# Optimization experiments

Hardware: AMD Instinct MI355X
Metric: run time of the kernel (lower is better)

Reference implementation:

```python
import jax, jax.numpy as jnp
import numpy as np

DIM = 512
NUM_HEADS = 8
HEAD_DIM = DIM // NUM_HEADS
SCALE = HEAD_DIM ** -0.5


def setup_inputs() -> dict:
    key = jax.random.key(0)
    k_x, k_qkv, k_proj, k_pb = jax.random.split(key, 4)
    x = jax.random.normal(k_x, (2, 4096, DIM), dtype=jnp.float32)
    # nn.Linear weights: stored as [out, in]; qkv_bias=False so no qkv bias.
    w_qkv = jax.random.normal(k_qkv, (3 * DIM, DIM), dtype=jnp.float32) * (DIM ** -0.5)
    w_proj = jax.random.normal(k_proj, (DIM, DIM), dtype=jnp.float32) * (DIM ** -0.5)
    b_proj = jax.random.normal(k_pb, (DIM,), dtype=jnp.float32) * 0.01
    return {"x": x, "w_qkv": w_qkv, "w_proj": w_proj, "b_proj": b_proj}


def reference(x, w_qkv, w_proj, b_proj):
    B, N, D = x.shape
    H, Hd = NUM_HEADS, HEAD_DIM
    # qkv: [B, N, 3D] -> [3, B, H, N, Hd]
    qkv = (x @ w_qkv.T).reshape(B, N, 3, H, Hd).transpose(2, 0, 3, 1, 4)
    q, k, v = qkv[0], qkv[1], qkv[2]
    # Naive full attention matrix in fp32 (matches original non-fused path).
    attn = jnp.einsum('bhqd,bhkd->bhqk', q, k) * SCALE
    attn = jax.nn.softmax(attn, axis=-1)
    out = jnp.einsum('bhqk,bhkd->bhqd', attn, v)
    out = out.transpose(0, 2, 1, 3).reshape(B, N, D)
    return out @ w_proj.T + b_proj
```

## Files before the change

### kernel.cpp

```cpp
#include <hip/hip_runtime.h>
#include <stdint.h>

#define SEQ   4096
#define DIMM  512
#define HDIM  64
#define NH    8
#define ROWS  8192
#define QKVN  1536

typedef __attribute__((ext_vector_type(8))) __bf16 bf16x8;
typedef __attribute__((ext_vector_type(4))) float  f32x4;
typedef __attribute__((ext_vector_type(2))) uint32_t u32x2;

__device__ __forceinline__ uint32_t cvtpk(float lo, float hi) {
  uint32_t w;
  asm("v_cvt_pk_bf16_f32 %0, %1, %2" : "=v"(w) : "v"(lo), "v"(hi));
  return w;
}

__device__ __forceinline__ f32x4 mfma16(bf16x8 a, bf16x8 b, f32x4 c) {
  return __builtin_amdgcn_mfma_f32_16x16x32_bf16(a, b, c, 0, 0, 0);
}

#if __has_builtin(__builtin_amdgcn_exp2f)
#define EXP2F(x) __builtin_amdgcn_exp2f(x)
#else
#define EXP2F(x) exp2f(x)
#endif

__device__ __forceinline__ void gld16(const void* g, void* l) {
  __builtin_amdgcn_global_load_lds(
      (const __attribute__((address_space(1))) uint32_t*)g,
      (__attribute__((address_space(3))) uint32_t*)l, 16, 0, 0);
}

#define X4  (ROWS * DIMM / 4)
#define Q4  (QKVN * DIMM / 4)
#define P4  (DIMM * DIMM / 4)

__global__ __launch_bounds__(256) void cvt_kernel(
    const float* __restrict__ x, const float* __restrict__ wq,
    const float* __restrict__ wp, uint16_t* __restrict__ xb,
    uint16_t* __restrict__ wqb, uint16_t* __restrict__ wpb) {
  int idx = blockIdx.x * 256 + threadIdx.x;
  const float* src; uint16_t* dst; int i4;
  if (idx < X4)            { src = x;  dst = xb;  i4 = idx; }
  else if (idx < X4 + Q4)  { src = wq; dst = wqb; i4 = idx - X4; }
  else                     { src = wp; dst = wpb; i4 = idx - X4 - Q4; }
  float4 v = ((const float4*)src)[i4];
  uint2 o;
  o.x = cvtpk(v.x, v.y);
  o.y = cvtpk(v.z, v.w);
  ((uint2*)dst)[i4] = o;
}

__device__ __forceinline__ void gemm_core(
    const uint16_t* __restrict__ A, const uint16_t* __restrict__ B,
    uint16_t* As, uint16_t* Bs, f32x4 acc[4][4]) {
  const int tid = threadIdx.x;
  const int lane = tid & 63, wave = tid >> 6;
  const int quad = lane >> 4, l16 = lane & 15;
  const int wr = (wave & 1) * 64, wc = (wave >> 1) * 64;
  const int bm = blockIdx.x, bn = blockIdx.y;
  const int sw = (l16 >> 1) & 3;

  for (int kt = 0; kt < DIMM / 32; ++kt) {
#pragma unroll
    for (int it = 0; it < 2; ++it) {
      int L = it * 256 + tid;
      int r = L >> 2, c = L & 3;
      int gc = c ^ ((r >> 1) & 3);
      int ldsoff = (it * 256 + (tid & ~63)) * 16;
      gld16((const char*)A + ((size_t)(bm * 128 + r) * DIMM + kt * 32) * 2 + gc * 16,
            (char*)As + ldsoff);
      gld16((const char*)B + ((size_t)(bn * 128 + r) * DIMM + kt * 32) * 2 + gc * 16,
            (char*)Bs + ldsoff);
    }
    __syncthreads();
    bf16x8 af[4], bfr[4];
#pragma unroll
    for (int i = 0; i < 4; ++i)
      af[i] = *(const bf16x8*)(As + (wr + i * 16 + l16) * 32 + ((quad ^ sw) * 8));
#pragma unroll
    for (int j = 0; j < 4; ++j)
      bfr[j] = *(const bf16x8*)(Bs + (wc + j * 16 + l16) * 32 + ((quad ^ sw) * 8));
#pragma unroll
    for (int i = 0; i < 4; ++i)
#pragma unroll
      for (int j = 0; j < 4; ++j)
        acc[i][j] = mfma16(af[i], bfr[j], acc[i][j]);
    __syncthreads();
  }
}

__global__ __launch_bounds__(256, 2) void qkv_gemm(
    const uint16_t* __restrict__ xb, const uint16_t* __restrict__ wqb,
    uint16_t* __restrict__ qd, uint16_t* __restrict__ kd,
    uint16_t* __restrict__ vt) {
  __shared__ __align__(16) uint16_t As[128 * 32];
  __shared__ __align__(16) uint16_t Bs[128 * 32];
  f32x4 acc[4][4];
#pragma unroll
  for (int i = 0; i < 4; ++i)
#pragma unroll
    for (int j = 0; j < 4; ++j) acc[i][j] = f32x4{0.f, 0.f, 0.f, 0.f};

  gemm_core(xb, wqb, As, Bs, acc);

  const int lane = threadIdx.x & 63, wave = threadIdx.x >> 6;
  const int quad = lane >> 4, l16 = lane & 15;
  const int wr = (wave & 1) * 64, wc = (wave >> 1) * 64;
  const float qscale = 0.125f * 1.44269504f;
#pragma unroll
  for (int i = 0; i < 4; ++i) {
    int m0 = blockIdx.x * 128 + wr + i * 16 + quad * 4;
    int b = m0 >> 12, n0 = m0 & 4095;
#pragma unroll
    for (int j = 0; j < 4; ++j) {
      int jc = blockIdx.y * 128 + wc + j * 16 + l16;
      int region = jc >> 9;
      int h = (jc >> 6) & 7, hd = jc & 63;
      int bh = (b << 3) | h;
      if (region == 0) {
        uint32_t w01 = cvtpk(acc[i][j][0] * qscale, acc[i][j][1] * qscale);
        uint32_t w23 = cvtpk(acc[i][j][2] * qscale, acc[i][j][3] * qscale);
        size_t rb = ((size_t)bh * SEQ + n0) * HDIM + hd;
        qd[rb]            = (uint16_t)w01;
        qd[rb + HDIM]     = (uint16_t)(w01 >> 16);
        qd[rb + 2 * HDIM] = (uint16_t)w23;
        qd[rb + 3 * HDIM] = (uint16_t)(w23 >> 16);
      } else if (region == 1) {
        uint32_t w01 = cvtpk(acc[i][j][0], acc[i][j][1]);
        uint32_t w23 = cvtpk(acc[i][j][2], acc[i][j][3]);
        size_t rb = ((size_t)bh * SEQ + n0) * HDIM + hd;
        kd[rb]            = (uint16_t)w01;
        kd[rb + HDIM]     = (uint16_t)(w01 >> 16);
        kd[rb + 2 * HDIM] = (uint16_t)w23;
        kd[rb + 3 * HDIM] = (uint16_t)(w23 >> 16);
      } else {
        uint2 pk;
        pk.x = cvtpk(acc[i][j][0], acc[i][j][1]);
        pk.y = cvtpk(acc[i][j][2], acc[i][j][3]);
        *(uint2*)(vt + ((size_t)bh * HDIM + hd) * SEQ + n0) = pk;
      }
    }
  }
}

__global__ __launch_bounds__(512, 4) void attn_kernel(
    const uint16_t* __restrict__ qd, const uint16_t* __restrict__ kd,
    const uint16_t* __restrict__ vt, uint16_t* __restrict__ ao) {
  __shared__ __align__(16) uint16_t Ks[128 * 64];
  __shared__ __align__(16) uint16_t Vs[64 * 128];
  __shared__ __align__(16) uint16_t Ps[8][32 * 64];

  const int tid = threadIdx.x, lane = tid & 63, wave = tid >> 6;
  const int quad = lane >> 4, l16 = lane & 15;
  const int pair = wave >> 1, khalf = wave & 1;
  const int wid = blockIdx.x;
  const int xcd = wid & 7, slot = wid >> 3;
  const int bh = xcd + 8 * (slot & 1);
  const int qt = slot >> 1;
  const size_t base_qk = (size_t)bh * SEQ * HDIM;
  const size_t base_v  = (size_t)bh * HDIM * SEQ;
  const int sw7 = l16 & 7;
  char* Pw = (char*)Ps + wave * 4096;

  bf16x8 qf[2][2];
#pragma unroll
  for (int it2 = 0; it2 < 2; ++it2)
#pragma unroll
    for (int kh = 0; kh < 2; ++kh)
      qf[it2][kh] = *(const bf16x8*)(qd + base_qk +
          (size_t)(qt * 128 + pair * 32 + it2 * 16 + l16) * HDIM + kh * 32 + quad * 8);

  f32x4 O[2][4];
  float lsum[2] = {0.f, 0.f};
#pragma unroll
  for (int a = 0; a < 2; ++a)
#pragma unroll
    for (int d = 0; d < 4; ++d) O[a][d] = f32x4{0.f, 0.f, 0.f, 0.f};

  for (int kt = 0; kt < SEQ / 128; ++kt) {
#pragma unroll
    for (int it = 0; it < 2; ++it) {
      int L = it * 512 + tid;
      int ldsoff = (it * 512 + (tid & ~63)) * 16;
      int rk = L >> 3, ck = L & 7;
      int gck = ck ^ (rk & 7);
      gld16((const char*)kd + (base_qk + (size_t)(kt * 128 + rk) * HDIM) * 2 + gck * 16,
            (char*)Ks + ldsoff);
      int rv = L >> 4, cv = L & 15;
      int gcv = cv ^ (rv & 15);
      gld16((const char*)vt + (base_v + (size_t)rv * SEQ + (size_t)kt * 128) * 2 + gcv * 16,
            (char*)Vs + ldsoff);
    }
    __syncthreads();

    bf16x8 kf[4][2];
#pragma unroll
    for (int jh = 0; jh < 4; ++jh) {
      int jf = khalf * 4 + jh;
      const uint16_t* krow = Ks + (jf * 16 + l16) * 64;
      kf[jh][0] = *(const bf16x8*)(krow + ((quad ^ sw7) * 8));
      kf[jh][1] = *(const bf16x8*)(krow + (((4 + quad) ^ sw7) * 8));
    }
    f32x4 P[4][2];
    __builtin_amdgcn_s_setprio(1);
#pragma unroll
    for (int jh = 0; jh < 4; ++jh)
#pragma unroll
      for (int it2 = 0; it2 < 2; ++it2) {
        f32x4 s = f32x4{0.f, 0.f, 0.f, 0.f};
        s = mfma16(kf[jh][0], qf[it2][0], s);
        s = mfma16(kf[jh][1], qf[it2][1], s);
        P[jh][it2] = s;
      }
    __builtin_amdgcn_s_setprio(0);

#pragma unroll
    for (int jh = 0; jh < 4; ++jh)
#pragma unroll
      for (int it2 = 0; it2 < 2; ++it2) {
        float p0 = EXP2F(P[jh][it2][0]);
        float p1 = EXP2F(P[jh][it2][1]);
        float p2 = EXP2F(P[jh][it2][2]);
        float p3 = EXP2F(P[jh][it2][3]);
        lsum[it2] += (p0 + p1) + (p2 + p3);
        u32x2 pk;
        pk.x = cvtpk(p0, p1);
        pk.y = cvtpk(p2, p3);
        int c16 = (jh * 2 + (quad >> 1)) ^ sw7;
        *(u32x2*)(Pw + (it2 * 16 + l16) * 128 + c16 * 16 + (quad & 1) * 8) = pk;
      }

#pragma unroll
    for (int kp = 0; kp < 2; ++kp) {
      bf16x8 pb[2];
#pragma unroll
      for (int it2 = 0; it2 < 2; ++it2)
        pb[it2] = *(const bf16x8*)(Pw + (it2 * 16 + l16) * 128 +
                                   (((kp * 4 + quad) ^ sw7) * 16));
      bf16x8 va[4];
#pragma unroll
      for (int dl = 0; dl < 4; ++dl)
        va[dl] = *(const bf16x8*)((const char*)Vs + (dl * 16 + l16) * 256 +
                                  (((khalf * 8 + kp * 4 + quad) ^ l16) & 15) * 16);
      __builtin_amdgcn_s_setprio(1);
#pragma unroll
      for (int it2 = 0; it2 < 2; ++it2)
#pragma unroll
        for (int dl = 0; dl < 4; ++dl)
          O[it2][dl] = mfma16(va[dl], pb[it2], O[it2][dl]);
      __builtin_amdgcn_s_setprio(0);
    }
    __syncthreads();
  }

  if (!(wave & 1)) {
    f32x4* ob = (f32x4*)((char*)Ps + wave * 4096);
#pragma unroll
    for (int it2 = 0; it2 < 2; ++it2)
#pragma unroll
      for (int dl = 0; dl < 4; ++dl)
        ob[(it2 * 4 + dl) * 64 + lane] = O[it2][dl];
    float2* lb = (float2*)((char*)Ks + pair * 512);
    lb[lane] = make_float2(lsum[0], lsum[1]);
  }
  __syncthreads();
  if (wave & 1) {
    const f32x4* ob = (const f32x4*)((char*)Ps + (wave - 1) * 4096);
    float2 lp = ((const float2*)((char*)Ks + pair * 512))[lane];
    lsum[0] += lp.x; lsum[1] += lp.y;
#pragma unroll
    for (int it2 = 0; it2 < 2; ++it2)
#pragma unroll
      for (int dl = 0; dl < 4; ++dl)
        O[it2][dl] += ob[(it2 * 4 + dl) * 64 + lane];

    const int b = bh >> 3, h = bh & 7;
#pragma unroll
    for (int it2 = 0; it2 < 2; ++it2) {
      float l = lsum[it2];
      l += __shfl_xor(l, 16);
      l += __shfl_xor(l, 32);
      float inv = 1.0f / l;
      int q = qt * 128 + pair * 32 + it2 * 16 + l16;
      size_t rowbase = ((size_t)(b * SEQ + q)) * DIMM + h * HDIM;
#pragma unroll
      for (int dl = 0; dl < 4; ++dl) {
        uint2 pk;
        pk.x = cvtpk(O[it2][dl][0] * inv, O[it2][dl][1] * inv);
        pk.y = cvtpk(O[it2][dl][2] * inv, O[it2][dl][3] * inv);
        *(uint2*)(ao + rowbase + dl * 16 + quad * 4) = pk;
      }
    }
  }
}

__global__ __launch_bounds__(256, 2) void proj_gemm(
    const uint16_t* __restrict__ ao, const uint16_t* __restrict__ wpb,
    const float* __restrict__ bprj, float* __restrict__ out) {
  __shared__ __align__(16) uint16_t As[128 * 32];
  __shared__ __align__(16) uint16_t Bs[128 * 32];
  f32x4 acc[4][4];
#pragma unroll
  for (int i = 0; i < 4; ++i)
#pragma unroll
    for (int j = 0; j < 4; ++j) acc[i][j] = f32x4{0.f, 0.f, 0.f, 0.f};

  gemm_core(ao, wpb, As, Bs, acc);

  const int lane = threadIdx.x & 63, wave = threadIdx.x >> 6;
  const int quad = lane >> 4, l16 = lane & 15;
  const int wr = (wave & 1) * 64, wc = (wave >> 1) * 64;
#pragma unroll
  for (int i = 0; i < 4; ++i) {
    int m0 = blockIdx.x * 128 + wr + i * 16 + quad * 4;
#pragma unroll
    for (int j = 0; j < 4; ++j) {
      int jc = blockIdx.y * 128 + wc + j * 16 + l16;
      float bias = bprj[jc];
#pragma unroll
      for (int r = 0; r < 4; ++r)
        out[(size_t)(m0 + r) * DIMM + jc] = acc[i][j][r] + bias;
    }
  }
}

extern "C" void kernel_launch(void* const* d_in, const int* in_sizes, int n_in,
                              void* d_out, int out_size, void* d_ws, size_t ws_size,
                              hipStream_t stream) {
  const float* x     = (const float*)d_in[0];
  const float* wqkv  = (const float*)d_in[1];
  const float* wproj = (const float*)d_in[2];
  const float* bproj = (const float*)d_in[3];

  char* ws = (char*)d_ws;
  uint16_t* xb  = (uint16_t*)(ws + 0);
  uint16_t* wqb = (uint16_t*)(ws + 8388608);
  uint16_t* wpb = (uint16_t*)(ws + 9961472);
  uint16_t* qd  = (uint16_t*)(ws + 10485760);
  uint16_t* kd  = (uint16_t*)(ws + 18874368);
  uint16_t* vt  = (uint16_t*)(ws + 27262976);
  uint16_t* ao  = (uint16_t*)(ws + 35651584);

  cvt_kernel<<<(X4 + Q4 + P4) / 256, 256, 0, stream>>>(x, wqkv, wproj, xb, wqb, wpb);
  qkv_gemm<<<dim3(64, 12), 256, 0, stream>>>(xb, wqb, qd, kd, vt);
  attn_kernel<<<512, 512, 0, stream>>>(qd, kd, vt, ao);
  proj_gemm<<<dim3(64, 4), 256, 0, stream>>>(ao, wpb, bproj, (float*)d_out);
}
```

Before: 183.2 us.

## Double-buffer LDS tiles and keep P in registers via 16x16x16 MFMA

Both GEMMs and the attention kernel now double-buffer their LDS tiles. The next tile's global-to-LDS load is issued right after the barrier, so it overlaps compute on the current tile, and one barrier per iteration is dropped. In attention, the softmax probabilities are packed straight into registers and consumed by a 16x16x16 bf16 MFMA, removing the P round-trip through LDS; the freed Ps space goes toward the extra K/V buffers. The GEMMs also raise the launch-bounds occupancy hint to 4 blocks and add setprio around the MFMA block. The trade-offs are more LDS per block and more, smaller MFMA instructions on the PV step.

```diff
diff --git a/kernel.cpp b/kernel.cpp
--- a/kernel.cpp
+++ b/kernel.cpp
@@ -9,7 +9,9 @@
 #define QKVN  1536
 
 typedef __attribute__((ext_vector_type(8))) __bf16 bf16x8;
+typedef __attribute__((ext_vector_type(4))) __bf16 bf16x4;
 typedef __attribute__((ext_vector_type(4))) float  f32x4;
+typedef __attribute__((ext_vector_type(4))) short  s16x4;
 typedef __attribute__((ext_vector_type(2))) uint32_t u32x2;
 
 __device__ __forceinline__ uint32_t cvtpk(float lo, float hi) {
@@ -20,6 +22,20 @@
 
 __device__ __forceinline__ f32x4 mfma16(bf16x8 a, bf16x8 b, f32x4 c) {
   return __builtin_amdgcn_mfma_f32_16x16x32_bf16(a, b, c, 0, 0, 0);
+}
+
+__device__ __forceinline__ f32x4 pv_mfma(s16x4 a, s16x4 b, f32x4 c) {
+#if __has_builtin(__builtin_amdgcn_mfma_f32_16x16x16bf16_1k)
+  return __builtin_amdgcn_mfma_f32_16x16x16bf16_1k(a, b, c, 0, 0, 0);
+#elif __has_builtin(__builtin_amdgcn_mfma_f32_16x16x16_bf16)
+  return __builtin_amdgcn_mfma_f32_16x16x16_bf16(
+      __builtin_bit_cast(bf16x4, a), __builtin_bit_cast(bf16x4, b), c, 0, 0, 0);
+#else
+  f32x4 d = c;
+  asm volatile("v_mfma_f32_16x16x16_bf16 %0, %1, %2, %3"
+               : "=v"(d) : "v"(a), "v"(b), "0"(d));
+  return d;
+#endif
 }
 
 #if __has_builtin(__builtin_amdgcn_exp2f)
@@ -56,7 +72,7 @@
 
 __device__ __forceinline__ void gemm_core(
     const uint16_t* __restrict__ A, const uint16_t* __restrict__ B,
-    uint16_t* As, uint16_t* Bs, f32x4 acc[4][4]) {
+    uint16_t (*As)[128 * 32], uint16_t (*Bs)[128 * 32], f32x4 acc[4][4]) {
   const int tid = threadIdx.x;
   const int lane = tid & 63, wave = tid >> 6;
   const int quad = lane >> 4, l16 = lane & 15;
@@ -64,7 +80,7 @@
   const int bm = blockIdx.x, bn = blockIdx.y;
   const int sw = (l16 >> 1) & 3;
 
-  for (int kt = 0; kt < DIMM / 32; ++kt) {
+  auto stage = [&](int buf, int kt) {
 #pragma unroll
     for (int it = 0; it < 2; ++it) {
       int L = it * 256 + tid;
@@ -72,33 +88,41 @@
       int gc = c ^ ((r >> 1) & 3);
       int ldsoff = (it * 256 + (tid & ~63)) * 16;
       gld16((const char*)A + ((size_t)(bm * 128 + r) * DIMM + kt * 32) * 2 + gc * 16,
-            (char*)As + ldsoff);
+            (char*)As[buf] + ldsoff);
       gld16((const char*)B + ((size_t)(bn * 128 + r) * DIMM + kt * 32) * 2 + gc * 16,
-            (char*)Bs + ldsoff);
-    }
+            (char*)Bs[buf] + ldsoff);
+    }
+  };
+
+  stage(0, 0);
+  for (int kt = 0; kt < DIMM / 32; ++kt) {
+    const int cur = kt & 1;
     __syncthreads();
+    if (kt < DIMM / 32 - 1) stage(cur ^ 1, kt + 1);
+
     bf16x8 af[4], bfr[4];
 #pragma unroll
     for (int i = 0; i < 4; ++i)
-      af[i] = *(const bf16x8*)(As + (wr + i * 16 + l16) * 32 + ((quad ^ sw) * 8));
+      af[i] = *(const bf16x8*)(As[cur] + (wr + i * 16 + l16) * 32 + ((quad ^ sw) * 8));
 #pragma unroll
     for (int j = 0; j < 4; ++j)
-      bfr[j] = *(const bf16x8*)(Bs + (wc + j * 16 + l16) * 32 + ((quad ^ sw) * 8));
+      bfr[j] = *(const bf16x8*)(Bs[cur] + (wc + j * 16 + l16) * 32 + ((quad ^ sw) * 8));
+    __builtin_amdgcn_s_setprio(1);
 #pragma unroll
     for (int i = 0; i < 4; ++i)
 #pragma unroll
       for (int j = 0; j < 4; ++j)
         acc[i][j] = mfma16(af[i], bfr[j], acc[i][j]);
-    __syncthreads();
-  }
-}
-
-__global__ __launch_bounds__(256, 2) void qkv_gemm(
+    __builtin_amdgcn_s_setprio(0);
+  }
+}
+
+__global__ __launch_bounds__(256, 4) void qkv_gemm(
     const uint16_t* __restrict__ xb, const uint16_t* __restrict__ wqb,
     uint16_t* __restrict__ qd, uint16_t* __restrict__ kd,
     uint16_t* __restrict__ vt) {
-  __shared__ __align__(16) uint16_t As[128 * 32];
-  __shared__ __align__(16) uint16_t Bs[128 * 32];
+  __shared__ __align__(16) uint16_t As[2][128 * 32];
+  __shared__ __align__(16) uint16_t Bs[2][128 * 32];
   f32x4 acc[4][4];
 #pragma unroll
   for (int i = 0; i < 4; ++i)
@@ -150,9 +174,8 @@
 __global__ __launch_bounds__(512, 4) void attn_kernel(
     const uint16_t* __restrict__ qd, const uint16_t* __restrict__ kd,
     const uint16_t* __restrict__ vt, uint16_t* __restrict__ ao) {
-  __shared__ __align__(16) uint16_t Ks[128 * 64];
-  __shared__ __align__(16) uint16_t Vs[64 * 128];
-  __shared__ __align__(16) uint16_t Ps[8][32 * 64];
+  __shared__ __align__(16) uint16_t Ks[2][128 * 64];
+  __shared__ __align__(16) uint16_t Vs[2][64 * 128];
 
   const int tid = threadIdx.x, lane = tid & 63, wave = tid >> 6;
   const int quad = lane >> 4, l16 = lane & 15;
@@ -164,24 +187,8 @@
   const size_t base_qk = (size_t)bh * SEQ * HDIM;
   const size_t base_v  = (size_t)bh * HDIM * SEQ;
   const int sw7 = l16 & 7;
-  char* Pw = (char*)Ps + wave * 4096;
-
-  bf16x8 qf[2][2];
-#pragma unroll
-  for (int it2 = 0; it2 < 2; ++it2)
-#pragma unroll
-    for (int kh = 0; kh < 2; ++kh)
-      qf[it2][kh] = *(const bf16x8*)(qd + base_qk +
-          (size_t)(qt * 128 + pair * 32 + it2 * 16 + l16) * HDIM + kh * 32 + quad * 8);
-
-  f32x4 O[2][4];
-  float lsum[2] = {0.f, 0.f};
-#pragma unroll
-  for (int a = 0; a < 2; ++a)
-#pragma unroll
-    for (int d = 0; d < 4; ++d) O[a][d] = f32x4{0.f, 0.f, 0.f, 0.f};
-
-  for (int kt = 0; kt < SEQ / 128; ++kt) {
+
+  auto stage = [&](int buf, int kt) {
 #pragma unroll
     for (int it = 0; it < 2; ++it) {
       int L = it * 512 + tid;
@@ -189,88 +196,102 @@
       int rk = L >> 3, ck = L & 7;
       int gck = ck ^ (rk & 7);
       gld16((const char*)kd + (base_qk + (size_t)(kt * 128 + rk) * HDIM) * 2 + gck * 16,
-            (char*)Ks + ldsoff);
+            (char*)Ks[buf] + ldsoff);
       int rv = L >> 4, cv = L & 15;
       int gcv = cv ^ (rv & 15);
       gld16((const char*)vt + (base_v + (size_t)rv * SEQ + (size_t)kt * 128) * 2 + gcv * 16,
-            (char*)Vs + ldsoff);
-    }
+            (char*)Vs[buf] + ldsoff);
+    }
+  };
+
+  bf16x8 qf[2][2];
+#pragma unroll
+  for (int it2 = 0; it2 < 2; ++it2)
+#pragma unroll
+    for (int kh = 0; kh < 2; ++kh)
+      qf[it2][kh] = *(const bf16x8*)(qd + base_qk +
+          (size_t)(qt * 128 + pair * 32 + it2 * 16 + l16) * HDIM + kh * 32 + quad * 8);
+
+  f32x4 O[2][4];
+  float lsum[2] = {0.f, 0.f};
+#pragma unroll
+  for (int a = 0; a < 2; ++a)
+#pragma unroll
+    for (int d = 0; d < 4; ++d) O[a][d] = f32x4{0.f, 0.f, 0.f, 0.f};
+
+  stage(0, 0);
+  for (int kt = 0; kt < SEQ / 128; ++kt) {
+    const int cur = kt & 1;
     __syncthreads();
+    if (kt < SEQ / 128 - 1) stage(cur ^ 1, kt + 1);
 
     bf16x8 kf[4][2];
 #pragma unroll
     for (int jh = 0; jh < 4; ++jh) {
       int jf = khalf * 4 + jh;
-      const uint16_t* krow = Ks + (jf * 16 + l16) * 64;
+      const uint16_t* krow = Ks[cur] + (jf * 16 + l16) * 64;
       kf[jh][0] = *(const bf16x8*)(krow + ((quad ^ sw7) * 8));
       kf[jh][1] = *(const bf16x8*)(krow + (((4 + quad) ^ sw7) * 8));
     }
-    f32x4 P[4][2];
-    __builtin_amdgcn_s_setprio(1);
-#pragma unroll
-    for (int jh = 0; jh < 4; ++jh)
+
+#pragma unroll
+    for (int jh = 0; jh < 4; ++jh) {
+      f32x4 P[2];
+      __builtin_amdgcn_s_setprio(1);
 #pragma unroll
       for (int it2 = 0; it2 < 2; ++it2) {
         f32x4 s = f32x4{0.f, 0.f, 0.f, 0.f};
         s = mfma16(kf[jh][0], qf[it2][0], s);
         s = mfma16(kf[jh][1], qf[it2][1], s);
-        P[jh][it2] = s;
+        P[it2] = s;
       }
-    __builtin_amdgcn_s_setprio(0);
-
-#pragma unroll
-    for (int jh = 0; jh < 4; ++jh)
+      __builtin_amdgcn_s_setprio(0);
+
+      s16x4 pb[2];
 #pragma unroll
       for (int it2 = 0; it2 < 2; ++it2) {
-        float p0 = EXP2F(P[jh][it2][0]);
-        float p1 = EXP2F(P[jh][it2][1]);
-        float p2 = EXP2F(P[jh][it2][2]);
-        float p3 = EXP2F(P[jh][it2][3]);
+        float p0 = EXP2F(P[it2][0]);
+        float p1 = EXP2F(P[it2][1]);
+        float p2 = EXP2F(P[it2][2]);
+        float p3 = EXP2F(P[it2][3]);
         lsum[it2] += (p0 + p1) + (p2 + p3);
-        u32x2 pk;
-        pk.x = cvtpk(p0, p1);
-        pk.y = cvtpk(p2, p3);
-        int c16 = (jh * 2 + (quad >> 1)) ^ sw7;
-        *(u32x2*)(Pw + (it2 * 16 + l16) * 128 + c16 * 16 + (quad & 1) * 8) = pk;
+        u32x2 t;
+        t.x = cvtpk(p0, p1);
+        t.y = cvtpk(p2, p3);
+        pb[it2] = __builtin_bit_cast(s16x4, t);
       }
 
-#pragma unroll
-    for (int kp = 0; kp < 2; ++kp) {
-      bf16x8 pb[2];
+      s16x4 va[4];
+#pragma unroll
+      for (int dl = 0; dl < 4; ++dl)
+        va[dl] = *(const s16x4*)((const char*)Vs[cur] + (dl * 16 + l16) * 256 +
+                  (((8 * khalf + 2 * jh + (quad >> 1)) ^ l16) & 15) * 16 +
+                  (quad & 1) * 8);
+      __builtin_amdgcn_s_setprio(1);
 #pragma unroll
       for (int it2 = 0; it2 < 2; ++it2)
-        pb[it2] = *(const bf16x8*)(Pw + (it2 * 16 + l16) * 128 +
-                                   (((kp * 4 + quad) ^ sw7) * 16));
-      bf16x8 va[4];
-#pragma unroll
-      for (int dl = 0; dl < 4; ++dl)
-        va[dl] = *(const bf16x8*)((const char*)Vs + (dl * 16 + l16) * 256 +
-                                  (((khalf * 8 + kp * 4 + quad) ^ l16) & 15) * 16);
-      __builtin_amdgcn_s_setprio(1);
-#pragma unroll
-      for (int it2 = 0; it2 < 2; ++it2)
 #pragma unroll
         for (int dl = 0; dl < 4; ++dl)
-          O[it2][dl] = mfma16(va[dl], pb[it2], O[it2][dl]);
+          O[it2][dl] = pv_mfma(va[dl], pb[it2], O[it2][dl]);
       __builtin_amdgcn_s_setprio(0);
     }
-    __syncthreads();
-  }
-
+  }
+
+  __syncthreads();
   if (!(wave & 1)) {
-    f32x4* ob = (f32x4*)((char*)Ps + wave * 4096);
+    f32x4* ob = (f32x4*)((char*)Ks + pair * 8192);
 #pragma unroll
     for (int it2 = 0; it2 < 2; ++it2)
 #pragma unroll
       for (int dl = 0; dl < 4; ++dl)
         ob[(it2 * 4 + dl) * 64 + lane] = O[it2][dl];
-    float2* lb = (float2*)((char*)Ks + pair * 512);
+    float2* lb = (float2*)((char*)Vs + pair * 512);
     lb[lane] = make_float2(lsum[0], lsum[1]);
   }
   __syncthreads();
   if (wave & 1) {
-    const f32x4* ob = (const f32x4*)((char*)Ps + (wave - 1) * 4096);
-    float2 lp = ((const float2*)((char*)Ks + pair * 512))[lane];
+    const f32x4* ob = (const f32x4*)((char*)Ks + pair * 8192);
+    float2 lp = ((const float2*)((char*)Vs + pair * 512))[lane];
     lsum[0] += lp.x; lsum[1] += lp.y;
 #pragma unroll
     for (int it2 = 0; it2 < 2; ++it2)
@@ -298,11 +319,11 @@
   }
 }
 
-__global__ __launch_bounds__(256, 2) void proj_gemm(
+__global__ __launch_bounds__(256, 4) void proj_gemm(
     const uint16_t* __restrict__ ao, const uint16_t* __restrict__ wpb,
     const float* __restrict__ bprj, float* __restrict__ out) {
-  __shared__ __align__(16) uint16_t As[128 * 32];
-  __shared__ __align__(16) uint16_t Bs[128 * 32];
+  __shared__ __align__(16) uint16_t As[2][128 * 32];
+  __shared__ __align__(16) uint16_t Bs[2][128 * 32];
   f32x4 acc[4][4];
 #pragma unroll
   for (int i = 0; i < 4; ++i)
```

After: 192.8 us. 5.2% more time.
